# Optimization experiments

Measured on AMD Instinct MI355X. Metric: run time of the kernel, lower is better.

The kernel has to match this reference:

```python
import jax, jax.numpy as jnp
import numpy as np

NUM_CLASSES = 5532  # matches __init__ default


def setup_inputs() -> dict:
    key = jax.random.key(0)
    k1, k2 = jax.random.split(key)
    N, F = 131072, 256
    Q = NUM_CLASSES * 2  # num_classes * number_of_instance
    return {
        "features": jax.random.normal(k1, (N, F), dtype=jnp.float32),
        "pid_labels": jax.random.randint(k2, (N,), 0, NUM_CLASSES),
        "large_batch_queue": jnp.zeros((Q, F), dtype=jnp.float32),
        "queue_label": jnp.zeros((Q,), dtype=jnp.float32),
        "tail": 0,
    }


def _update(features, queue, qlabel, pid_labels, tail):
    """Functional equivalent of the torch in-place circular-queue update.

    torch.unique returns labels in sorted order, so the loop writes the
    per-label means for sorted present labels >= 0 at positions
    tail, tail+1, ... (mod queue_size). We compute all per-label means with
    one segment reduction and scatter them in a single pass.
    """
    Q = queue.shape[0]
    # map negative (unlabeled) ids to an overflow segment that is discarded
    lbl = jnp.where(pid_labels >= 0, pid_labels, NUM_CLASSES)
    sums = jax.ops.segment_sum(features, lbl, num_segments=NUM_CLASSES + 1)[:NUM_CLASSES]
    counts = jax.ops.segment_sum(
        jnp.ones(lbl.shape, jnp.float32), lbl, num_segments=NUM_CLASSES + 1
    )[:NUM_CLASSES]
    means = sums / jnp.maximum(counts, 1.0)[:, None]  # [num_classes, F]
    present = counts > 0
    # rank of each present label among sorted present labels
    rank = jnp.cumsum(present.astype(jnp.int32)) - 1
    # circular write position; absent labels get out-of-range index Q -> dropped
    pos = jnp.where(present, (tail + rank) % Q, Q)
    new_queue = queue.at[pos].set(means, mode="drop")
    new_label = qlabel.at[pos].set(jnp.arange(NUM_CLASSES, dtype=jnp.float32), mode="drop")
    return new_queue, new_label


def reference(features, pid_labels, large_batch_queue, queue_label, tail):
    # original update happens under torch.no_grad()
    feats = jax.lax.stop_gradient(features)
    return _update(feats, large_batch_queue, queue_label, pid_labels, tail)
```

## Files before the change

kernel.cpp:

```cpp
#include <hip/hip_runtime.h>
#include <hip/hip_bf16.h>

#define NCLS 5532
#define FDIM 256

__global__ void k_count(const int* __restrict__ labels, int n, int* __restrict__ counts) {
    int i = blockIdx.x * blockDim.x + threadIdx.x;
    int st = gridDim.x * blockDim.x;
    for (; i < n; i += st) {
        int l = labels[i];
        if (l >= 0 && l < NCLS) atomicAdd(&counts[l], 1);
    }
}

__global__ __launch_bounds__(256) void k_scan(const int* __restrict__ counts,
                                              int* __restrict__ offsets,
                                              int* __restrict__ rank) {
    const int T = 256;
    const int CH = (NCLS + T - 1) / T;
    __shared__ int s_c[T], s_p[T];
    int t = threadIdx.x;
    int base = t * CH;
    int cs = 0, ps = 0;
    for (int j = 0; j < CH; ++j) {
        int i = base + j;
        if (i < NCLS) { int c = counts[i]; cs += c; ps += (c > 0); }
    }
    s_c[t] = cs; s_p[t] = ps;
    __syncthreads();
    for (int off = 1; off < T; off <<= 1) {
        int vc = (t >= off) ? s_c[t - off] : 0;
        int vp = (t >= off) ? s_p[t - off] : 0;
        __syncthreads();
        s_c[t] += vc; s_p[t] += vp;
        __syncthreads();
    }
    int ec = (t == 0) ? 0 : s_c[t - 1];
    int ep = (t == 0) ? 0 : s_p[t - 1];
    for (int j = 0; j < CH; ++j) {
        int i = base + j;
        if (i < NCLS) {
            offsets[i] = ec; rank[i] = ep;
            int c = counts[i];
            ec += c; ep += (c > 0);
        }
    }
}

__global__ void k_scatter(const int* __restrict__ labels, int n,
                          const int* __restrict__ offsets,
                          int* __restrict__ cursor,
                          int* __restrict__ rowlist) {
    int i = blockIdx.x * blockDim.x + threadIdx.x;
    int st = gridDim.x * blockDim.x;
    for (; i < n; i += st) {
        int l = labels[i];
        if (l >= 0 && l < NCLS) {
            int j = atomicAdd(&cursor[l], 1);
            rowlist[offsets[l] + j] = i;
        }
    }
}

__global__ __launch_bounds__(256) void k_means(const float* __restrict__ feats,
                                               const int* __restrict__ counts,
                                               const int* __restrict__ offsets,
                                               const int* __restrict__ rank,
                                               const int* __restrict__ rowlist,
                                               const int* __restrict__ tailp,
                                               float* __restrict__ outq,
                                               float* __restrict__ outl,
                                               int Q) {
    int c = blockIdx.x;
    int cnt = counts[c];
    if (cnt == 0) return;
    int t = threadIdx.x;
    int lane = t & 63;
    int w = t >> 6;
    int off = offsets[c];
    float4 acc = make_float4(0.f, 0.f, 0.f, 0.f);
    for (int i = w; i < cnt; i += 4) {
        int r = rowlist[off + i];
        const float4 v = ((const float4*)(feats + (size_t)r * FDIM))[lane];
        acc.x += v.x; acc.y += v.y; acc.z += v.z; acc.w += v.w;
    }
    __shared__ float4 s_acc[3][64];
    if (w > 0) s_acc[w - 1][lane] = acc;
    __syncthreads();
    if (w == 0) {
        for (int k = 0; k < 3; ++k) {
            float4 v = s_acc[k][lane];
            acc.x += v.x; acc.y += v.y; acc.z += v.z; acc.w += v.w;
        }
        float inv = 1.0f / (float)cnt;
        int pos = (tailp[0] + rank[c]) % Q;
        if (pos < 0) pos += Q;
        float4 m = make_float4(acc.x * inv, acc.y * inv, acc.z * inv, acc.w * inv);
        ((float4*)(outq + (size_t)pos * FDIM))[lane] = m;
        if (lane == 0) outl[pos] = (float)c;
    }
}

extern "C" void kernel_launch(void* const* d_in, const int* in_sizes, int n_in,
                              void* d_out, int out_size, void* d_ws, size_t ws_size,
                              hipStream_t stream) {
    const float* feats  = (const float*)d_in[0];
    const int*   labels = (const int*)d_in[1];
    const float* queue  = (const float*)d_in[2];
    const float* qlabel = (const float*)d_in[3];
    const int*   tailp  = (const int*)d_in[4];
    int N  = in_sizes[1];
    int QF = in_sizes[2];
    int Q  = in_sizes[3];
    float* outq = (float*)d_out;
    float* outl = outq + (size_t)QF;

    int* counts  = (int*)d_ws;
    int* cursor  = counts + NCLS;
    int* offsets = cursor + NCLS;
    int* rank    = offsets + NCLS;
    int* rowlist = rank + NCLS;

    hipMemsetAsync(counts, 0, 2 * NCLS * sizeof(int), stream);
    hipMemcpyAsync(outq, queue, (size_t)QF * sizeof(float), hipMemcpyDeviceToDevice, stream);
    hipMemcpyAsync(outl, qlabel, (size_t)Q * sizeof(float), hipMemcpyDeviceToDevice, stream);

    k_count<<<512, 256, 0, stream>>>(labels, N, counts);
    k_scan<<<1, 256, 0, stream>>>(counts, offsets, rank);
    k_scatter<<<512, 256, 0, stream>>>(labels, N, offsets, cursor, rowlist);
    k_means<<<NCLS, 256, 0, stream>>>(feats, counts, offsets, rank, rowlist, tailp, outq, outl, Q);
}
```

Measured before the change: 258.1 us.

## Map one wavefront per class in means kernel and vectorize label loads

New measurement: 263.8 us. 1.02x slower.

```diff
diff --git a/kernel.cpp b/kernel.cpp
--- a/kernel.cpp
+++ b/kernel.cpp
@@ -4,13 +4,14 @@
 #define NCLS 5532
 #define FDIM 256
 
-__global__ void k_count(const int* __restrict__ labels, int n, int* __restrict__ counts) {
+__global__ void k_hist(const int* __restrict__ labels, int n4, int* __restrict__ counts) {
     int i = blockIdx.x * blockDim.x + threadIdx.x;
-    int st = gridDim.x * blockDim.x;
-    for (; i < n; i += st) {
-        int l = labels[i];
-        if (l >= 0 && l < NCLS) atomicAdd(&counts[l], 1);
-    }
+    if (i >= n4) return;
+    int4 l = ((const int4*)labels)[i];
+    if (l.x >= 0 && l.x < NCLS) atomicAdd(&counts[l.x], 1);
+    if (l.y >= 0 && l.y < NCLS) atomicAdd(&counts[l.y], 1);
+    if (l.z >= 0 && l.z < NCLS) atomicAdd(&counts[l.z], 1);
+    if (l.w >= 0 && l.w < NCLS) atomicAdd(&counts[l.w], 1);
 }
 
 __global__ __launch_bounds__(256) void k_scan(const int* __restrict__ counts,
@@ -47,19 +48,18 @@
     }
 }
 
-__global__ void k_scatter(const int* __restrict__ labels, int n,
+__global__ void k_scatter(const int* __restrict__ labels, int n4,
                           const int* __restrict__ offsets,
                           int* __restrict__ cursor,
                           int* __restrict__ rowlist) {
     int i = blockIdx.x * blockDim.x + threadIdx.x;
-    int st = gridDim.x * blockDim.x;
-    for (; i < n; i += st) {
-        int l = labels[i];
-        if (l >= 0 && l < NCLS) {
-            int j = atomicAdd(&cursor[l], 1);
-            rowlist[offsets[l] + j] = i;
-        }
-    }
+    if (i >= n4) return;
+    int4 l = ((const int4*)labels)[i];
+    int r = i * 4;
+    if (l.x >= 0 && l.x < NCLS) rowlist[offsets[l.x] + atomicAdd(&cursor[l.x], 1)] = r;
+    if (l.y >= 0 && l.y < NCLS) rowlist[offsets[l.y] + atomicAdd(&cursor[l.y], 1)] = r + 1;
+    if (l.z >= 0 && l.z < NCLS) rowlist[offsets[l.z] + atomicAdd(&cursor[l.z], 1)] = r + 2;
+    if (l.w >= 0 && l.w < NCLS) rowlist[offsets[l.w] + atomicAdd(&cursor[l.w], 1)] = r + 3;
 }
 
 __global__ __launch_bounds__(256) void k_means(const float* __restrict__ feats,
@@ -71,34 +71,40 @@
                                                float* __restrict__ outq,
                                                float* __restrict__ outl,
                                                int Q) {
-    int c = blockIdx.x;
+    int c = blockIdx.x * 4 + (threadIdx.x >> 6);
+    if (c >= NCLS) return;
     int cnt = counts[c];
     if (cnt == 0) return;
-    int t = threadIdx.x;
-    int lane = t & 63;
-    int w = t >> 6;
+    int lane = threadIdx.x & 63;
     int off = offsets[c];
+    const float4* f4 = (const float4*)feats;
     float4 acc = make_float4(0.f, 0.f, 0.f, 0.f);
-    for (int i = w; i < cnt; i += 4) {
+    int i = 0;
+    for (; i + 4 <= cnt; i += 4) {
+        int r0 = rowlist[off + i];
+        int r1 = rowlist[off + i + 1];
+        int r2 = rowlist[off + i + 2];
+        int r3 = rowlist[off + i + 3];
+        float4 v0 = f4[(size_t)r0 * 64 + lane];
+        float4 v1 = f4[(size_t)r1 * 64 + lane];
+        float4 v2 = f4[(size_t)r2 * 64 + lane];
+        float4 v3 = f4[(size_t)r3 * 64 + lane];
+        acc.x += v0.x + v1.x + v2.x + v3.x;
+        acc.y += v0.y + v1.y + v2.y + v3.y;
+        acc.z += v0.z + v1.z + v2.z + v3.z;
+        acc.w += v0.w + v1.w + v2.w + v3.w;
+    }
+    for (; i < cnt; ++i) {
         int r = rowlist[off + i];
-        const float4 v = ((const float4*)(feats + (size_t)r * FDIM))[lane];
+        float4 v = f4[(size_t)r * 64 + lane];
         acc.x += v.x; acc.y += v.y; acc.z += v.z; acc.w += v.w;
     }
-    __shared__ float4 s_acc[3][64];
-    if (w > 0) s_acc[w - 1][lane] = acc;
-    __syncthreads();
-    if (w == 0) {
-        for (int k = 0; k < 3; ++k) {
-            float4 v = s_acc[k][lane];
-            acc.x += v.x; acc.y += v.y; acc.z += v.z; acc.w += v.w;
-        }
-        float inv = 1.0f / (float)cnt;
-        int pos = (tailp[0] + rank[c]) % Q;
-        if (pos < 0) pos += Q;
-        float4 m = make_float4(acc.x * inv, acc.y * inv, acc.z * inv, acc.w * inv);
-        ((float4*)(outq + (size_t)pos * FDIM))[lane] = m;
-        if (lane == 0) outl[pos] = (float)c;
-    }
+    float inv = 1.0f / (float)cnt;
+    int pos = (tailp[0] + rank[c]) % Q;
+    if (pos < 0) pos += Q;
+    float4 m = make_float4(acc.x * inv, acc.y * inv, acc.z * inv, acc.w * inv);
+    ((float4*)(outq + (size_t)pos * FDIM))[lane] = m;
+    if (lane == 0) outl[pos] = (float)c;
 }
 
 extern "C" void kernel_launch(void* const* d_in, const int* in_sizes, int n_in,
@@ -125,8 +131,9 @@
     hipMemcpyAsync(outq, queue, (size_t)QF * sizeof(float), hipMemcpyDeviceToDevice, stream);
     hipMemcpyAsync(outl, qlabel, (size_t)Q * sizeof(float), hipMemcpyDeviceToDevice, stream);
 
-    k_count<<<512, 256, 0, stream>>>(labels, N, counts);
+    int n4 = N / 4;
+    k_hist<<<(n4 + 255) / 256, 256, 0, stream>>>(labels, n4, counts);
     k_scan<<<1, 256, 0, stream>>>(counts, offsets, rank);
-    k_scatter<<<512, 256, 0, stream>>>(labels, N, offsets, cursor, rowlist);
-    k_means<<<NCLS, 256, 0, stream>>>(feats, counts, offsets, rank, rowlist, tailp, outq, outl, Q);
+    k_scatter<<<(n4 + 255) / 256, 256, 0, stream>>>(labels, n4, offsets, cursor, rowlist);
+    k_means<<<(NCLS + 3) / 4, 256, 0, stream>>>(feats, counts, offsets, rank, rowlist, tailp, outq, outl, Q);
 }
```
